# Performance work log

Hardware: AMD Instinct MI355X
Metric: run time of the kernel (lower is better)

## Reference

```python
import jax, jax.numpy as jnp
import numpy as np

N = 512    # hidden states
M = 4096   # emission symbols
B = 64     # batch
TMAX = 512 # max sequence length


def setup_inputs() -> dict:
    key = jax.random.key(0)
    k1, k2, k3, k4, k5 = jax.random.split(key, 5)
    x = jax.random.randint(k1, (B, TMAX), 0, M)                       # observations
    T = jax.random.randint(k2, (B,), 1, TMAX + 1)                     # lengths in [1, TMAX]
    emission_logits = jax.random.normal(k3, (N, M), dtype=jnp.float32)
    transition_logits = jax.random.normal(k4, (N, N), dtype=jnp.float32)
    prior_logits = jax.random.normal(k5, (N,), dtype=jnp.float32)
    return {
        "x": x,
        "T": T,
        "emission_logits": emission_logits,
        "transition_logits": transition_logits,
        "prior_logits": prior_logits,
    }


def reference(x, T, emission_logits, transition_logits, prior_logits):
    # Normalize once (the torch code recomputes log_softmax every step; same math).
    log_em = jax.nn.log_softmax(emission_logits, axis=1)      # (N, M), row-stochastic
    log_tr = jax.nn.log_softmax(transition_logits, axis=0)    # (N, N), column-stochastic: tr[j,k] = p(j|k)
    log_pri = jax.nn.log_softmax(prior_logits, axis=0)        # (N,)

    obs = log_em.T[x]                                         # (B, TMAX, N): log p(x_t | state)

    log_alpha0 = obs[:, 0, :] + log_pri                       # (B, N)

    def step(log_alpha, obs_t):
        # new[b, j] = obs_t[b, j] + logsumexp_k( log_tr[j, k] + log_alpha[b, k] )
        new = obs_t + jax.nn.logsumexp(log_alpha[:, None, :] + log_tr[None, :, :], axis=2)
        return new, new

    _, rest = jax.lax.scan(step, log_alpha0, jnp.swapaxes(obs[:, 1:, :], 0, 1))
    log_alpha = jnp.concatenate([log_alpha0[:, None, :], jnp.swapaxes(rest, 0, 1)], axis=1)  # (B, TMAX, N)

    log_sums = jax.nn.logsumexp(log_alpha, axis=2)            # (B, TMAX)
    log_probs = jnp.take_along_axis(log_sums, (T - 1)[:, None], axis=1)  # (B, 1)
    return log_probs
```

## Files before the change

kernel.cpp:

```cpp
#include <hip/hip_runtime.h>
#include <math.h>

#define HN 512
#define HM 4096
#define HB 64
#define HT 512

#if __has_builtin(__builtin_amdgcn_udot8)
  #define ENC_BIASED 0
  __device__ __forceinline__ int dot8q(unsigned int a, unsigned int b, int c){
    return (int)__builtin_amdgcn_udot8(a, b, (unsigned int)c, false);
  }
#elif __has_builtin(__builtin_amdgcn_sdot8)
  #define ENC_BIASED 1
  __device__ __forceinline__ int dot8q(unsigned int a, unsigned int b, int c){
    return __builtin_amdgcn_sdot8((int)a, (int)b, c, false);
  }
#else
  #define ENC_BIASED 0
  __device__ __forceinline__ int dot4u8f(unsigned int a, unsigned int b, int c){
#if __has_builtin(__builtin_amdgcn_sdot4)
    return __builtin_amdgcn_sdot4((int)a, (int)b, c, false);
#else
    c += (int)(a & 0xffu)       * (int)(b & 0xffu);
    c += (int)((a>>8) & 0xffu)  * (int)((b>>8) & 0xffu);
    c += (int)((a>>16) & 0xffu) * (int)((b>>16) & 0xffu);
    c += (int)(a>>24)           * (int)(b>>24);
    return c;
#endif
  }
  __device__ __forceinline__ int dot8q(unsigned int a, unsigned int b, int c){
    unsigned int al = a & 0x0F0F0F0Fu, ah = (a>>4) & 0x0F0F0F0Fu;
    unsigned int bl = b & 0x0F0F0F0Fu, bh = (b>>4) & 0x0F0F0F0Fu;
    c = dot4u8f(al, bl, c);
    return dot4u8f(ah, bh, c);
  }
#endif

__device__ __forceinline__ float rcpf(float x){
#if __has_builtin(__builtin_amdgcn_rcpf)
  return __builtin_amdgcn_rcpf(x);
#else
  return 1.0f / x;
#endif
}

__device__ __forceinline__ float wsum(float v){
  #pragma unroll
  for(int o=32;o>0;o>>=1) v += __shfl_xor(v,o,64);
  return v;
}
__device__ __forceinline__ float wmax(float v){
  #pragma unroll
  for(int o=32;o>0;o>>=1) v = fmaxf(v,__shfl_xor(v,o,64));
  return v;
}

__device__ __forceinline__ float blockSum512(float v, float* red, float* bc){
  v = wsum(v);
  if((threadIdx.x & 63)==0) red[threadIdx.x>>6] = v;
  __syncthreads();
  if(threadIdx.x < 64){
    float s = (threadIdx.x<8)? red[threadIdx.x] : 0.0f;
    #pragma unroll
    for(int o=4;o>0;o>>=1) s += __shfl_xor(s,o,64);
    if(threadIdx.x==0) *bc = s;
  }
  __syncthreads();
  return *bc;
}
__device__ __forceinline__ float blockMax512(float v, float* red, float* bc){
  v = wmax(v);
  if((threadIdx.x & 63)==0) red[threadIdx.x>>6] = v;
  __syncthreads();
  if(threadIdx.x < 64){
    float s = (threadIdx.x<8)? red[threadIdx.x] : -INFINITY;
    #pragma unroll
    for(int o=4;o>0;o>>=1) s = fmaxf(s, __shfl_xor(s,o,64));
    if(threadIdx.x==0) *bc = s;
  }
  __syncthreads();
  return *bc;
}

__device__ __forceinline__ unsigned short f2bf(float f){
  unsigned int u = __float_as_uint(f);
  unsigned int r = (u + 0x7fffu + ((u>>16)&1u)) >> 16;
  return (unsigned short)r;
}
__device__ __forceinline__ float bf2f(unsigned int w){ return __uint_as_float(w<<16); }


__global__ __launch_bounds__(512) void k_em_lse(const float* __restrict__ em, float* __restrict__ em_lse){
  __shared__ float red[8]; __shared__ float bc;
  int r = blockIdx.x;
  const float* row = em + (size_t)r*HM;
  float mx = -INFINITY;
  for(int i=threadIdx.x;i<HM;i+=512) mx = fmaxf(mx, row[i]);
  mx = blockMax512(mx, red, &bc);
  float s = 0.f;
  for(int i=threadIdx.x;i<HM;i+=512) s += expf(row[i]-mx);
  s = blockSum512(s, red, &bc);
  if(threadIdx.x==0) em_lse[r] = mx + logf(s);
}

__global__ __launch_bounds__(512) void k_pri(const float* __restrict__ pri, float* __restrict__ P, float* __restrict__ pric){
  __shared__ float red[8]; __shared__ float bc;
  int j = threadIdx.x;
  float v = pri[j];
  float mx = blockMax512(v, red, &bc);
  float w = expf(v-mx);
  float s = blockSum512(w, red, &bc);
  P[j] = w;
  if(j==0) *pric = -logf(s);
}

__global__ __launch_bounds__(256) void k_em_tab(const float* __restrict__ em, const float* __restrict__ em_lse,
                                                unsigned short* __restrict__ emT){
  __shared__ unsigned short tile[64][66];
  __shared__ float lsl[64];
  int m0 = blockIdx.x*64, j0 = blockIdx.y*64;
  int tx = threadIdx.x & 63, ty = threadIdx.x >> 6;
  if(threadIdx.x < 64) lsl[threadIdx.x] = em_lse[j0 + threadIdx.x];
  __syncthreads();
  #pragma unroll
  for(int r=0;r<16;r++){
    int jl = ty*16 + r;
    float v = em[(size_t)(j0+jl)*HM + m0 + tx];
    tile[jl][tx] = f2bf(expf(v - lsl[jl]));
  }
  __syncthreads();
  #pragma unroll
  for(int r=0;r<16;r++){
    int ml = ty*16 + r;
    emT[(size_t)(m0+ml)*HN + j0 + tx] = tile[tx][ml];
  }
}

__global__ __launch_bounds__(512) void k_trcol(const float* __restrict__ tr,
                                               float* __restrict__ cmax, float* __restrict__ csum){
  __shared__ float red[8]; __shared__ float bc;
  int k = blockIdx.x, j = threadIdx.x;
  float v = tr[(size_t)j*HN + k];
  float mx = blockMax512(v, red, &bc);
  float s  = blockSum512(expf(v-mx), red, &bc);
  if(j==0){ cmax[k] = mx; csum[k] = s; }
}

__global__ __launch_bounds__(512) void k_trrow(const float* __restrict__ tr,
                                               const float* __restrict__ cmax, const float* __restrict__ csum,
                                               unsigned char* __restrict__ TQ4,
                                               float* __restrict__ rscale, float* __restrict__ rbar,
                                               unsigned short* __restrict__ tsumq){
  __shared__ float red[8]; __shared__ float bc;
  int j = blockIdx.x, k = threadIdx.x;
  float v = expf(tr[(size_t)j*HN + k] - cmax[k]) / csum[k];
  float rm = blockMax512(v, red, &bc);
  int q = __float2int_rn(v * (15.0f/rm));
  float rs = blockSum512(v, red, &bc);
  float qs = blockSum512((float)q, red, &bc);
  float wq = wsum((float)q);
  int qn = __shfl_down(q, 1, 64);
  if((k & 1)==0){
#if ENC_BIASED
    unsigned char by = (unsigned char)(((q-8)&0xF) | (((qn-8)&0xF)<<4));
#else
    unsigned char by = (unsigned char)((q&0xF) | ((qn&0xF)<<4));
#endif
    TQ4[(size_t)j*256 + ((k>>5)<<4) + ((k&31)>>1)] = by;
  }
  if((k&63)==0) tsumq[j*8 + (k>>6)] = (unsigned short)(int)wq;
  if(k==0){
    rscale[j] = rm * (1.0f/15.0f);
    rbar[j]   = rs - (rm * (1.0f/15.0f)) * qs;
  }
}

__global__ __launch_bounds__(512)
void k_fwd(const int* __restrict__ x, const int* __restrict__ Tl,
           const unsigned short* __restrict__ emTu,
           const float* __restrict__ P, const float* __restrict__ pric,
           const float* __restrict__ rscaleG, const float* __restrict__ rbarG,
           const unsigned short* __restrict__ tsumqG,
           const uint4* __restrict__ TQd4,
           float* __restrict__ out){
  extern __shared__ char smem[];
  uint4*         apl4  = (uint4*)smem;
  unsigned char* aplB  = (unsigned char*)smem;
  float*         sigS  = (float*)(smem + 512);
  float*         sumS  = (float*)(smem + 576);
  float*         aqS   = (float*)(smem + 640);
  float*         rawS  = (float*)(smem + 704);
  int*           xls   = (int*)(smem + 768);
  float*         rscL  = (float*)(smem + 2816);
  float*         rbarL = (float*)(smem + 4864);
  unsigned short* tsumL= (unsigned short*)(smem + 6912);

  const int t = threadIdx.x, b = blockIdx.x, w = t>>6, L = t&63;
  const int j = t;

  unsigned int trq[64];
  #pragma unroll
  for(int q=0;q<16;q++) ((uint4*)trq)[q] = TQd4[j*16 + q];
  #pragma unroll
  for(int r=0;r<64;r++) asm volatile("" : "+v"(trq[r]));

  xls[t]   = x[b*HT + t];
  rscL[t]  = rscaleG[t];
  rbarL[t] = rbarG[t];
  for(int d=t; d<2048; d+=512) ((unsigned int*)tsumL)[d] = ((const unsigned int*)tsumqG)[d];
  int Tb = Tl[b];
  __syncthreads();

  int m = xls[0];
  float e0 = bf2f((unsigned)emTu[(size_t)m*HN + j]);
  float nvr = e0 * P[j];
  {
    float s = wsum(nvr);
    if(L==0) rawS[w] = s;
  }
  __syncthreads();
  float4 q0 = ((float4*)rawS)[0], q1 = ((float4*)rawS)[1];
  float S0 = ((q0.x+q0.y)+(q0.z+q0.w))+((q1.x+q1.y)+(q1.z+q1.w));
  float c_acc = pric[0] + __logf(S0);
  float nvd = nvr * rcpf(S0);
  {
    float Mw = fmaxf(wmax(nvd), 1e-30f);
    float sig = Mw * (1.0f/15.0f);
    int aq = __float2int_rn(nvd * (15.0f * rcpf(Mw)));
    float Sw = wsum(nvd);
#if ENC_BIASED
    float AqSw = wsum((float)aq);
#endif
    int aqn = __shfl_xor(aq, 1, 64);
    if((j&1)==0){
#if ENC_BIASED
      aplB[256 + (j>>1)] = (unsigned char)(((aq-8)&0xF) | (((aqn-8)&0xF)<<4));
#else
      aplB[256 + (j>>1)] = (unsigned char)((aq&0xF) | ((aqn&0xF)<<4));
#endif
    }
    if(L==0){
      sigS[8+w] = sig; sumS[8+w] = Sw;
#if ENC_BIASED
      aqS[8+w] = AqSw;
#endif
    }
  }
  int mn = xls[(Tb>1)?1:0];
  float eC = bf2f((unsigned)emTu[(size_t)mn*HN + j]);
  const float rsc = rscL[j], rbr = rbarL[j];

  for(int tt=1; tt<Tb; tt++){
    __syncthreads();
    const int rb = (tt & 1), wb = rb ^ 1;

    int acc[8];
    #pragma unroll
    for(int i=0;i<8;i++) acc[i] = 0;
    const uint4* aplR = apl4 + 16*rb;
    #pragma unroll
    for(int c=0;c<16;c++){
      uint4 A = aplR[c];
      int wi = c>>1;
      acc[wi] = dot8q(trq[4*c+0], A.x, acc[wi]);
      acc[wi] = dot8q(trq[4*c+1], A.y, acc[wi]);
      acc[wi] = dot8q(trq[4*c+2], A.z, acc[wi]);
      acc[wi] = dot8q(trq[4*c+3], A.w, acc[wi]);
    }

    float4 g0 = ((float4*)(sumS + 8*rb))[0], g1 = ((float4*)(sumS + 8*rb))[1];
    float Sp = ((g0.x+g0.y)+(g0.z+g0.w))+((g1.x+g1.y)+(g1.z+g1.w));
    if(tt > 1) c_acc += __logf(Sp);
    float d_inv = rcpf(Sp);
    float abar  = Sp * (1.0f/512.0f);
    float4 s0 = ((float4*)(sigS + 8*rb))[0], s1 = ((float4*)(sigS + 8*rb))[1];
    float sg[8] = {s0.x,s0.y,s0.z,s0.w,s1.x,s1.y,s1.z,s1.w};

    float Af = 0.f;
#if ENC_BIASED
    {
      float4 a0 = ((float4*)(aqS + 8*rb))[0], a1 = ((float4*)(aqS + 8*rb))[1];
      float av[8] = {a0.x,a0.y,a0.z,a0.w,a1.x,a1.y,a1.z,a1.w};
      uint4 tq = ((const uint4*)tsumL)[j];
      int ts[8] = {(int)(tq.x&0xffff),(int)(tq.x>>16),(int)(tq.y&0xffff),(int)(tq.y>>16),
                   (int)(tq.z&0xffff),(int)(tq.z>>16),(int)(tq.w&0xffff),(int)(tq.w>>16)};
      #pragma unroll
      for(int i=0;i<8;i++)
        Af += sg[i] * (float)(acc[i] + 8*(ts[i] + (int)av[i]) - 4096);
    }
#else
    #pragma unroll
    for(int i=0;i<8;i++) Af += sg[i] * (float)acc[i];
#endif
    float D = rsc * Af + abar * rbr;
    nvd = fmaxf(D * eC * d_inv, 0.0f);

    int tn = (tt+1 < HT)? tt+1 : HT-1;
    mn = xls[tn];
    float eN = bf2f((unsigned)emTu[(size_t)mn*HN + j]);

    float Mw = fmaxf(wmax(nvd), 1e-30f);
    float sig = Mw * (1.0f/15.0f);
    int aq = __float2int_rn(nvd * (15.0f * rcpf(Mw)));
    float Sw = wsum(nvd);
#if ENC_BIASED
    float AqSw = wsum((float)aq);
#endif
    int aqn = __shfl_xor(aq, 1, 64);
    if((j&1)==0){
#if ENC_BIASED
      aplB[256*wb + (j>>1)] = (unsigned char)(((aq-8)&0xF) | (((aqn-8)&0xF)<<4));
#else
      aplB[256*wb + (j>>1)] = (unsigned char)((aq&0xF) | ((aqn&0xF)<<4));
#endif
    }
    if(L==0){
      sigS[8*wb+w] = sig; sumS[8*wb+w] = Sw;
#if ENC_BIASED
      aqS[8*wb+w] = AqSw;
#endif
    }
    eC = eN;
  }

  __syncthreads();
  {
    const int fb = (Tb & 1);
    float4 g0 = ((float4*)(sumS + 8*fb))[0], g1 = ((float4*)(sumS + 8*fb))[1];
    float Sf = ((g0.x+g0.y)+(g0.z+g0.w))+((g1.x+g1.y)+(g1.z+g1.w));
    if(t==0) out[b] = c_acc + __logf(Sf);
  }
}

extern "C" void kernel_launch(void* const* d_in, const int* in_sizes, int n_in,
                              void* d_out, int out_size, void* d_ws, size_t ws_size,
                              hipStream_t stream){
  const int*   x   = (const int*)d_in[0];
  const int*   T   = (const int*)d_in[1];
  const float* em  = (const float*)d_in[2];
  const float* tr  = (const float*)d_in[3];
  const float* pri = (const float*)d_in[4];
  float* out = (float*)d_out;

  char* ws = (char*)d_ws;
  float* em_lse = (float*)ws;
  float* P      = (float*)(ws + 2048);
  float* pric   = (float*)(ws + 4096);
  float* cmax   = (float*)(ws + 8192);
  float* csum   = (float*)(ws + 10240);
  float* rscale = (float*)(ws + 12288);
  float* rbar   = (float*)(ws + 14336);
  unsigned short* tsumq = (unsigned short*)(ws + 16384);
  unsigned short* emT = (unsigned short*)(ws + 24576);
  unsigned char*  TQ4 = (unsigned char*)(ws + 24576 + (size_t)HM*HN*2);

  k_em_lse<<<HN, 512, 0, stream>>>(em, em_lse);
  k_pri   <<<1,  512, 0, stream>>>(pri, P, pric);
  k_trcol <<<HN, 512, 0, stream>>>(tr, cmax, csum);
  k_trrow <<<HN, 512, 0, stream>>>(tr, cmax, csum, TQ4, rscale, rbar, tsumq);
  k_em_tab<<<dim3(HM/64, HN/64), 256, 0, stream>>>(em, em_lse, emT);

  const int lds_bytes = 15104;
  (void)hipFuncSetAttribute((const void*)k_fwd, hipFuncAttributeMaxDynamicSharedMemorySize, lds_bytes);
  k_fwd<<<HB, 512, lds_bytes, stream>>>(x, T, emT, P, pric, rscale, rbar, tsumq,
                                        (const uint4*)TQ4, out);
}
```

Measured before the change: 578.3 us.

## Split quantized transition rows between registers and LDS, broadcast alpha via readlane

Each thread now keeps only half of its 4-bit transition row in registers and stores the other half in a swizzled LDS region, which cuts VGPR pressure. The packed alpha vector and per-wave statistics are read once per step as one dword per lane and broadcast with readlane, replacing the repeated uint4 and float4 LDS broadcast loads. Per-step scale terms (rscale, rbar, tsum) are held in registers. The cost is one extra LDS read stream for the stored half of the rows, many scalar readlane instructions per step, and a much larger LDS allocation.

```diff
diff --git a/kernel.cpp b/kernel.cpp
--- a/kernel.cpp
+++ b/kernel.cpp
@@ -35,6 +35,18 @@
     c = dot4u8f(al, bl, c);
     return dot4u8f(ah, bh, c);
   }
+#endif
+
+#if __has_builtin(__builtin_amdgcn_readlane)
+  __device__ __forceinline__ unsigned rdlaneu(unsigned v, int l){
+    return (unsigned)__builtin_amdgcn_readlane((int)v, l);
+  }
+  __device__ __forceinline__ float rdlanef(float v, int l){
+    return __int_as_float(__builtin_amdgcn_readlane(__float_as_int(v), l));
+  }
+#else
+  __device__ __forceinline__ unsigned rdlaneu(unsigned v, int l){ return (unsigned)__shfl((int)v, l, 64); }
+  __device__ __forceinline__ float rdlanef(float v, int l){ return __shfl(v, l, 64); }
 #endif
 
 __device__ __forceinline__ float rcpf(float x){
@@ -185,30 +197,26 @@
            const uint4* __restrict__ TQd4,
            float* __restrict__ out){
   extern __shared__ char smem[];
-  uint4*         apl4  = (uint4*)smem;
   unsigned char* aplB  = (unsigned char*)smem;
-  float*         sigS  = (float*)(smem + 512);
-  float*         sumS  = (float*)(smem + 576);
-  float*         aqS   = (float*)(smem + 640);
-  float*         rawS  = (float*)(smem + 704);
+  unsigned int*  aplD  = (unsigned int*)smem;
+  float*         statsF= (float*)(smem + 512);
   int*           xls   = (int*)(smem + 768);
-  float*         rscL  = (float*)(smem + 2816);
-  float*         rbarL = (float*)(smem + 4864);
-  unsigned short* tsumL= (unsigned short*)(smem + 6912);
+  uint4*         trH4  = (uint4*)(smem + 4096);
 
   const int t = threadIdx.x, b = blockIdx.x, w = t>>6, L = t&63;
   const int j = t;
 
-  unsigned int trq[64];
-  #pragma unroll
-  for(int q=0;q<16;q++) ((uint4*)trq)[q] = TQd4[j*16 + q];
-  #pragma unroll
-  for(int r=0;r<64;r++) asm volatile("" : "+v"(trq[r]));
-
-  xls[t]   = x[b*HT + t];
-  rscL[t]  = rscaleG[t];
-  rbarL[t] = rbarG[t];
-  for(int d=t; d<2048; d+=512) ((unsigned int*)tsumL)[d] = ((const unsigned int*)tsumqG)[d];
+  #pragma unroll
+  for(int c=0;c<8;c++) trH4[j*8 + (c ^ (j&7))] = TQd4[j*16 + 8 + c];
+  unsigned int trqR[32];
+  #pragma unroll
+  for(int q=0;q<8;q++) ((uint4*)trqR)[q] = TQd4[j*16 + q];
+  #pragma unroll
+  for(int r=0;r<32;r++) asm volatile("" : "+v"(trqR[r]));
+
+  xls[t] = x[b*HT + t];
+  const float rsc = rscaleG[j], rbr = rbarG[j];
+  const uint4 tq = *(const uint4*)(tsumqG + j*8);
   int Tb = Tl[b];
   __syncthreads();
 
@@ -217,11 +225,16 @@
   float nvr = e0 * P[j];
   {
     float s = wsum(nvr);
-    if(L==0) rawS[w] = s;
-  }
-  __syncthreads();
-  float4 q0 = ((float4*)rawS)[0], q1 = ((float4*)rawS)[1];
-  float S0 = ((q0.x+q0.y)+(q0.z+q0.w))+((q1.x+q1.y)+(q1.z+q1.w));
+    if(L==0) statsF[32 + 24 + w] = s;
+  }
+  __syncthreads();
+  float S0;
+  {
+    float sV = statsF[32 + (L&31)];
+    S0 = 0.f;
+    #pragma unroll
+    for(int i=0;i<8;i++) S0 += rdlanef(sV, 24+i);
+  }
   float c_acc = pric[0] + __logf(S0);
   float nvd = nvr * rcpf(S0);
   {
@@ -241,57 +254,65 @@
 #endif
     }
     if(L==0){
-      sigS[8+w] = sig; sumS[8+w] = Sw;
-#if ENC_BIASED
-      aqS[8+w] = AqSw;
+      statsF[32 + w] = sig; statsF[32 + 8 + w] = Sw;
+#if ENC_BIASED
+      statsF[32 + 16 + w] = AqSw;
 #endif
     }
   }
   int mn = xls[(Tb>1)?1:0];
   float eC = bf2f((unsigned)emTu[(size_t)mn*HN + j]);
-  const float rsc = rscL[j], rbr = rbarL[j];
 
   for(int tt=1; tt<Tb; tt++){
     __syncthreads();
     const int rb = (tt & 1), wb = rb ^ 1;
 
+    unsigned aV = aplD[rb*64 + L];
+    float    sV = statsF[rb*32 + (L&31)];
+
     int acc[8];
     #pragma unroll
     for(int i=0;i<8;i++) acc[i] = 0;
-    const uint4* aplR = apl4 + 16*rb;
-    #pragma unroll
-    for(int c=0;c<16;c++){
-      uint4 A = aplR[c];
-      int wi = c>>1;
-      acc[wi] = dot8q(trq[4*c+0], A.x, acc[wi]);
-      acc[wi] = dot8q(trq[4*c+1], A.y, acc[wi]);
-      acc[wi] = dot8q(trq[4*c+2], A.z, acc[wi]);
-      acc[wi] = dot8q(trq[4*c+3], A.w, acc[wi]);
-    }
-
-    float4 g0 = ((float4*)(sumS + 8*rb))[0], g1 = ((float4*)(sumS + 8*rb))[1];
-    float Sp = ((g0.x+g0.y)+(g0.z+g0.w))+((g1.x+g1.y)+(g1.z+g1.w));
+    #pragma unroll
+    for(int c=0;c<8;c++){
+      const int wi = c>>1;
+      #pragma unroll
+      for(int d=0;d<4;d++){
+        acc[wi] = dot8q(trqR[4*c+d], rdlaneu(aV, 4*c+d), acc[wi]);
+      }
+    }
+    #pragma unroll
+    for(int c=0;c<8;c++){
+      uint4 T = trH4[j*8 + (c ^ (j&7))];
+      const int wi = 4 + (c>>1);
+      acc[wi] = dot8q(T.x, rdlaneu(aV, 32+4*c+0), acc[wi]);
+      acc[wi] = dot8q(T.y, rdlaneu(aV, 32+4*c+1), acc[wi]);
+      acc[wi] = dot8q(T.z, rdlaneu(aV, 32+4*c+2), acc[wi]);
+      acc[wi] = dot8q(T.w, rdlaneu(aV, 32+4*c+3), acc[wi]);
+    }
+
+    float Sp = 0.f;
+    #pragma unroll
+    for(int i=0;i<8;i++) Sp += rdlanef(sV, 8+i);
     if(tt > 1) c_acc += __logf(Sp);
     float d_inv = rcpf(Sp);
     float abar  = Sp * (1.0f/512.0f);
-    float4 s0 = ((float4*)(sigS + 8*rb))[0], s1 = ((float4*)(sigS + 8*rb))[1];
-    float sg[8] = {s0.x,s0.y,s0.z,s0.w,s1.x,s1.y,s1.z,s1.w};
 
     float Af = 0.f;
 #if ENC_BIASED
     {
-      float4 a0 = ((float4*)(aqS + 8*rb))[0], a1 = ((float4*)(aqS + 8*rb))[1];
-      float av[8] = {a0.x,a0.y,a0.z,a0.w,a1.x,a1.y,a1.z,a1.w};
-      uint4 tq = ((const uint4*)tsumL)[j];
       int ts[8] = {(int)(tq.x&0xffff),(int)(tq.x>>16),(int)(tq.y&0xffff),(int)(tq.y>>16),
                    (int)(tq.z&0xffff),(int)(tq.z>>16),(int)(tq.w&0xffff),(int)(tq.w>>16)};
       #pragma unroll
-      for(int i=0;i<8;i++)
-        Af += sg[i] * (float)(acc[i] + 8*(ts[i] + (int)av[i]) - 4096);
-    }
-#else
-    #pragma unroll
-    for(int i=0;i<8;i++) Af += sg[i] * (float)acc[i];
+      for(int i=0;i<8;i++){
+        float sg = rdlanef(sV, i);
+        float av = rdlanef(sV, 16+i);
+        Af += sg * (float)(acc[i] + 8*(ts[i] + (int)av) - 4096);
+      }
+    }
+#else
+    #pragma unroll
+    for(int i=0;i<8;i++) Af += rdlanef(sV, i) * (float)acc[i];
 #endif
     float D = rsc * Af + abar * rbr;
     nvd = fmaxf(D * eC * d_inv, 0.0f);
@@ -316,9 +337,9 @@
 #endif
     }
     if(L==0){
-      sigS[8*wb+w] = sig; sumS[8*wb+w] = Sw;
-#if ENC_BIASED
-      aqS[8*wb+w] = AqSw;
+      statsF[wb*32 + w] = sig; statsF[wb*32 + 8 + w] = Sw;
+#if ENC_BIASED
+      statsF[wb*32 + 16 + w] = AqSw;
 #endif
     }
     eC = eN;
@@ -327,8 +348,10 @@
   __syncthreads();
   {
     const int fb = (Tb & 1);
-    float4 g0 = ((float4*)(sumS + 8*fb))[0], g1 = ((float4*)(sumS + 8*fb))[1];
-    float Sf = ((g0.x+g0.y)+(g0.z+g0.w))+((g1.x+g1.y)+(g1.z+g1.w));
+    float sV = statsF[fb*32 + (L&31)];
+    float Sf = 0.f;
+    #pragma unroll
+    for(int i=0;i<8;i++) Sf += rdlanef(sV, 8+i);
     if(t==0) out[b] = c_acc + __logf(Sf);
   }
 }
@@ -361,7 +384,7 @@
   k_trrow <<<HN, 512, 0, stream>>>(tr, cmax, csum, TQ4, rscale, rbar, tsumq);
   k_em_tab<<<dim3(HM/64, HN/64), 256, 0, stream>>>(em, em_lse, emT);
 
-  const int lds_bytes = 15104;
+  const int lds_bytes = 69632;
   (void)hipFuncSetAttribute((const void*)k_fwd, hipFuncAttributeMaxDynamicSharedMemorySize, lds_bytes);
   k_fwd<<<HB, 512, lds_bytes, stream>>>(x, T, emT, P, pric, rscale, rbar, tsumq,
                                         (const uint4*)TQ4, out);
```

After: 790.5 us. 1.37x slower.
